# Performance work log

Measured on AMD Instinct MI355X. Metric: run time of the kernel, lower is better.

Reference implementation:

```python
import jax, jax.numpy as jnp
import numpy as np

N_NODES = 100000
N_EDGES = 600000
N_GRAPHS = 512
F_IN = 128
F_HID = 128
F_OUT = 128


def setup_inputs() -> dict:
    key = jax.random.key(0)
    ks = jax.random.split(key, 10)
    x = jax.random.normal(ks[0], (N_NODES, F_IN), dtype=jnp.float32)
    edge_index = jax.random.randint(ks[1], (2, N_EDGES), 0, N_NODES, dtype=jnp.int64)
    batch = jnp.sort(jax.random.randint(ks[2], (N_NODES,), 0, N_GRAPHS, dtype=jnp.int64))
    s1 = 1.0 / np.sqrt(F_IN)
    s2 = 1.0 / np.sqrt(F_HID)
    s3 = 1.0 / np.sqrt(F_OUT)
    W1 = jax.random.uniform(ks[3], (F_IN, F_HID), jnp.float32, -s1, s1)
    b1 = jnp.zeros((F_HID,), jnp.float32)
    W2 = jax.random.uniform(ks[4], (F_HID, F_OUT), jnp.float32, -s2, s2)
    b2 = jnp.zeros((F_OUT,), jnp.float32)
    Wlin = jax.random.uniform(ks[5], (F_OUT, 1), jnp.float32, -s3, s3)
    blin = jax.random.uniform(ks[6], (1,), jnp.float32, -s3, s3)
    return {"x": x, "edge_index": edge_index, "batch": batch,
            "W1": W1, "b1": b1, "W2": W2, "b2": b2, "Wlin": Wlin, "blin": blin}


def reference(x, edge_index, batch, W1, b1, W2, b2, Wlin, blin):
    N = x.shape[0]
    # GCN normalization with self-loops: D^{-1/2} (A + I) D^{-1/2}
    loop = jnp.arange(N, dtype=edge_index.dtype)
    src = jnp.concatenate([edge_index[0], loop])  # [E + N]
    dst = jnp.concatenate([edge_index[1], loop])
    deg = jax.ops.segment_sum(jnp.ones_like(dst, dtype=x.dtype), dst, num_segments=N)
    dis = jnp.where(deg > 0, jax.lax.rsqrt(jnp.maximum(deg, 1.0)), 0.0)  # deg^{-1/2}
    norm = (dis[src] * dis[dst])[:, None]  # [E+N, 1] edge weights

    def gcn_conv(h, W, b):
        hW = h @ W                                      # [N, d_out]
        msgs = norm * hW[src]                           # gather + scale
        agg = jax.ops.segment_sum(msgs, dst, num_segments=N)  # scatter-add
        return agg + b

    h = jax.nn.relu(gcn_conv(x, W1, b1))
    h = gcn_conv(h, W2, b2)

    # global_mean_pool over graph ids
    counts = jax.ops.segment_sum(jnp.ones((N,), x.dtype), batch, num_segments=N_GRAPHS)
    pooled = jax.ops.segment_sum(h, batch, num_segments=N_GRAPHS)
    pooled = pooled / jnp.maximum(counts, 1.0)[:, None]  # [N_GRAPHS, F_OUT]

    # dropout is identity in eval mode
    return pooled @ Wlin + blin  # [N_GRAPHS, 1]
```

## Files before the change

kernel.cpp:

```cpp
#include <hip/hip_runtime.h>

#define F 128
#define CAP 32

typedef _Float16 f16x8 __attribute__((ext_vector_type(8)));
typedef float f32x4 __attribute__((ext_vector_type(4)));

__global__ __launch_bounds__(256) void k_gemm_mfma(const float* __restrict__ X,
                                                   const float* __restrict__ W1,
                                                   int* __restrict__ cnt,
                                                   _Float16* __restrict__ Yb, int N) {
    __shared__ _Float16 Bs[F * F];

    int tid = threadIdx.x;
    int g = blockIdx.x;

    int zrow = g * 128 + tid;
    if (tid < 128 && zrow < N) cnt[zrow] = 0;

    {
        int krow = tid >> 1;
        int n0 = (tid & 1) * 64;
        int t = krow >> 5, j = krow & 7, qa = (krow >> 3) & 3;
        const float* wp = &W1[krow * F + n0];
#pragma unroll
        for (int q4 = 0; q4 < 16; ++q4) {
            float4 w = *(const float4*)(wp + q4 * 4);
            int n = n0 + q4 * 4;
            int c = n >> 4;
            int m = n & 15;
            int ob = (t * 8 + c) * 512 + j;
            Bs[ob + (qa * 16 + m + 0) * 8] = (_Float16)w.x;
            Bs[ob + (qa * 16 + m + 1) * 8] = (_Float16)w.y;
            Bs[ob + (qa * 16 + m + 2) * 8] = (_Float16)w.z;
            Bs[ob + (qa * 16 + m + 3) * 8] = (_Float16)w.w;
        }
    }
    __syncthreads();

    int lane = tid & 63, wave = tid >> 6;
    int quad = lane >> 4, m = lane & 15;
    int r0 = g * 128 + wave * 32;

    f32x4 acc[2][8];
#pragma unroll
    for (int rt = 0; rt < 2; ++rt)
#pragma unroll
        for (int c = 0; c < 8; ++c) acc[rt][c] = (f32x4)0.0f;

    int ra = r0 + m;      if (ra >= N) ra = N - 1;
    int rb = r0 + 16 + m; if (rb >= N) rb = N - 1;
    const float* pxa = &X[(size_t)ra * F + quad * 8];
    const float* pxb = &X[(size_t)rb * F + quad * 8];

    float4 a0 = *(const float4*)pxa, a1 = *(const float4*)(pxa + 4);
    float4 a2 = *(const float4*)pxb, a3 = *(const float4*)(pxb + 4);

#pragma unroll 1
    for (int t = 0; t < 4; ++t) {
        const _Float16* bp = &Bs[t * 4096 + lane * 8];
        f16x8 B[8];
#pragma unroll
        for (int c = 0; c < 8; ++c) B[c] = *(const f16x8*)(bp + c * 512);

        float fa[8] = {a0.x, a0.y, a0.z, a0.w, a1.x, a1.y, a1.z, a1.w};
        float fb[8] = {a2.x, a2.y, a2.z, a2.w, a3.x, a3.y, a3.z, a3.w};
        f16x8 A0, A1;
#pragma unroll
        for (int j = 0; j < 8; ++j) {
            A0[j] = (_Float16)fa[j];
            A1[j] = (_Float16)fb[j];
        }
        if (t < 3) {
            a0 = *(const float4*)(pxa + (t + 1) * 32);
            a1 = *(const float4*)(pxa + (t + 1) * 32 + 4);
            a2 = *(const float4*)(pxb + (t + 1) * 32);
            a3 = *(const float4*)(pxb + (t + 1) * 32 + 4);
        }
#pragma unroll
        for (int c = 0; c < 8; ++c) {
            acc[0][c] = __builtin_amdgcn_mfma_f32_16x16x32_f16(A0, B[c], acc[0][c], 0, 0, 0);
            acc[1][c] = __builtin_amdgcn_mfma_f32_16x16x32_f16(A1, B[c], acc[1][c], 0, 0, 0);
        }
    }

#pragma unroll
    for (int rt = 0; rt < 2; ++rt) {
        int rbase = r0 + rt * 16 + quad * 4;
#pragma unroll
        for (int rr = 0; rr < 4; ++rr) {
            int row = rbase + rr;
            if (row < N) {
#pragma unroll
                for (int c = 0; c < 8; ++c)
                    Yb[(size_t)row * F + c * 16 + m] = (_Float16)acc[rt][c][rr];
            }
        }
    }
}

__global__ __launch_bounds__(256) void k_prep(const float* __restrict__ W2, const float* __restrict__ Wlin,
                                              const float* __restrict__ b2, const float* __restrict__ blin,
                                              const int* __restrict__ batch,
                                              const int* __restrict__ src, const int* __restrict__ dst,
                                              float* __restrict__ w2l, float* __restrict__ cconst,
                                              int* __restrict__ gstart, int* __restrict__ cnt,
                                              int* __restrict__ srcs, int N, int E, int G, int bG) {
    int bid = blockIdx.x;
    int tid = threadIdx.x;
    if (bid == 0) {
        __shared__ float sh[F];
        if (tid < F) {
            float s = 0.0f;
            for (int j = 0; j < F; j += 4) {
                float4 w = *(const float4*)&W2[tid * F + j];
                float4 l = *(const float4*)&Wlin[j];
                s += w.x * l.x + w.y * l.y + w.z * l.z + w.w * l.w;
            }
            w2l[tid] = s;
            sh[tid] = b2[tid] * Wlin[tid];
        }
        __syncthreads();
        if (tid == 0) {
            float c = blin[0];
            for (int j = 0; j < F; ++j) c += sh[j];
            *cconst = c;
        }
    } else if (bid <= bG) {
        int g = (bid - 1) * 256 + tid;
        if (g < G) {
            int lo = 0, hi = N;
            while (lo < hi) { int mid = (lo + hi) >> 1; if (batch[mid] < g) lo = mid + 1; else hi = mid; }
            gstart[g] = lo;
            if (g == 0) gstart[G] = N;
        }
    } else {
        int e = (bid - 1 - bG) * 256 + tid;
        if (e < E) {
            int s = src[e], d = dst[e];
            int slot = atomicAdd(&cnt[d], 1);
            if (slot < CAP) srcs[d * CAP + slot] = s;
        }
    }
}

__global__ __launch_bounds__(256) void k_agg_z(const _Float16* __restrict__ hWb,
                                               const int* __restrict__ cnt, const int* __restrict__ srcs,
                                               const float* __restrict__ bias, const float* __restrict__ w2l,
                                               float* __restrict__ zt, int N) {
    __shared__ int sdeg[32], snode[32], smapN[32], smapD[32];
    int tid = threadIdx.x;
    int nb = blockIdx.x * 32;
    if (tid < 32) {
        int n = nb + tid;
        sdeg[tid]  = (n < N) ? cnt[n] : 0x40000000;
        snode[tid] = (n < N) ? n : -1;
    }
    __syncthreads();
    if (tid < 32) {
        int v = sdeg[tid];
        int rank = 0;
#pragma unroll 8
        for (int j = 0; j < 32; ++j) {
            int vj = sdeg[j];
            rank += (vj < v) || (vj == v && j < tid);
        }
        smapN[rank] = snode[tid];
        smapD[rank] = sdeg[tid];
    }
    __syncthreads();
    int node = smapN[tid >> 3];
    if (node < 0) return;
    int dg = smapD[tid >> 3];
    float di = rsqrtf((float)dg + 1.0f);
    int lane = tid & 7;
    float s[16];
    {
        const _Float16* pr = &hWb[(size_t)node * F + lane * 16];
        f16x8 v0 = *(const f16x8*)pr;
        f16x8 v1 = *(const f16x8*)(pr + 8);
#pragma unroll
        for (int j = 0; j < 8; ++j) { s[j] = di * (float)v0[j]; s[8 + j] = di * (float)v1[j]; }
    }
    int du = min(dg, CAP);
    int e0 = node * CAP, e1 = e0 + du;
    int e = e0;
    for (; e + 4 <= e1; e += 4) {
        int i0 = srcs[e], i1 = srcs[e + 1], i2 = srcs[e + 2], i3 = srcs[e + 3];
        float w0 = rsqrtf((float)cnt[i0] + 1.0f);
        float w1 = rsqrtf((float)cnt[i1] + 1.0f);
        float w2 = rsqrtf((float)cnt[i2] + 1.0f);
        float w3 = rsqrtf((float)cnt[i3] + 1.0f);
        const _Float16* p0 = &hWb[(size_t)i0 * F + lane * 16];
        const _Float16* p1 = &hWb[(size_t)i1 * F + lane * 16];
        const _Float16* p2 = &hWb[(size_t)i2 * F + lane * 16];
        const _Float16* p3 = &hWb[(size_t)i3 * F + lane * 16];
        f16x8 a0 = *(const f16x8*)p0, b0 = *(const f16x8*)(p0 + 8);
        f16x8 a1 = *(const f16x8*)p1, b1 = *(const f16x8*)(p1 + 8);
        f16x8 a2 = *(const f16x8*)p2, b2 = *(const f16x8*)(p2 + 8);
        f16x8 a3 = *(const f16x8*)p3, b3 = *(const f16x8*)(p3 + 8);
#pragma unroll
        for (int j = 0; j < 8; ++j) {
            s[j]     = fmaf(w0, (float)a0[j], s[j]);
            s[j]     = fmaf(w1, (float)a1[j], s[j]);
            s[j]     = fmaf(w2, (float)a2[j], s[j]);
            s[j]     = fmaf(w3, (float)a3[j], s[j]);
            s[8 + j] = fmaf(w0, (float)b0[j], s[8 + j]);
            s[8 + j] = fmaf(w1, (float)b1[j], s[8 + j]);
            s[8 + j] = fmaf(w2, (float)b2[j], s[8 + j]);
            s[8 + j] = fmaf(w3, (float)b3[j], s[8 + j]);
        }
    }
    for (; e < e1; ++e) {
        int i0 = srcs[e];
        float w0 = rsqrtf((float)cnt[i0] + 1.0f);
        const _Float16* pr = &hWb[(size_t)i0 * F + lane * 16];
        f16x8 v0 = *(const f16x8*)pr;
        f16x8 v1 = *(const f16x8*)(pr + 8);
#pragma unroll
        for (int j = 0; j < 8; ++j) {
            s[j]     = fmaf(w0, (float)v0[j], s[j]);
            s[8 + j] = fmaf(w0, (float)v1[j], s[8 + j]);
        }
    }
    float p = 0.0f;
#pragma unroll
    for (int q = 0; q < 4; ++q) {
        float4 bb = *(const float4*)&bias[lane * 16 + q * 4];
        float4 ww = *(const float4*)&w2l[lane * 16 + q * 4];
        p += fmaxf(fmaf(di, s[q * 4 + 0], bb.x), 0.0f) * ww.x;
        p += fmaxf(fmaf(di, s[q * 4 + 1], bb.y), 0.0f) * ww.y;
        p += fmaxf(fmaf(di, s[q * 4 + 2], bb.z), 0.0f) * ww.z;
        p += fmaxf(fmaf(di, s[q * 4 + 3], bb.w), 0.0f) * ww.w;
    }
#pragma unroll
    for (int d = 1; d < 8; d <<= 1) p += __shfl_xor(p, d);
    if (lane == 0) zt[node] = di * p;
}

__global__ __launch_bounds__(256) void k_pool(const float* __restrict__ zt,
                                              const int* __restrict__ cnt, const int* __restrict__ srcs,
                                              const int* __restrict__ gstart, const float* __restrict__ cconst,
                                              const float* __restrict__ blin, float* __restrict__ out, int G) {
    int g = blockIdx.x;
    int g0 = gstart[g], g1 = gstart[g + 1];
    float acc = 0.0f;
    for (int n = g0 + threadIdx.x; n < g1; n += 256) {
        float s = zt[n];
        int dg = cnt[n];
        int du = min(dg, CAP);
        int e0 = n * CAP, e1 = e0 + du;
        int e = e0;
        for (; e + 4 <= e1; e += 4) {
            s += zt[srcs[e]] + zt[srcs[e + 1]] + zt[srcs[e + 2]] + zt[srcs[e + 3]];
        }
        for (; e < e1; ++e) s += zt[srcs[e]];
        acc += rsqrtf((float)dg + 1.0f) * s;
    }
#pragma unroll
    for (int d = 1; d < 64; d <<= 1) acc += __shfl_xor(acc, d);
    __shared__ float ws4[4];
    if ((threadIdx.x & 63) == 0) ws4[threadIdx.x >> 6] = acc;
    __syncthreads();
    if (threadIdx.x == 0) {
        float sum = ws4[0] + ws4[1] + ws4[2] + ws4[3];
        int c = g1 - g0;
        out[g] = (c > 0) ? (sum / (float)c + cconst[0]) : blin[0];
    }
}


extern "C" void kernel_launch(void* const* d_in, const int* in_sizes, int n_in,
                              void* d_out, int out_size, void* d_ws, size_t ws_size,
                              hipStream_t stream) {
    const float* x    = (const float*)d_in[0];
    const int*   ei   = (const int*)d_in[1];
    const int*   batch= (const int*)d_in[2];
    const float* W1   = (const float*)d_in[3];
    const float* b1   = (const float*)d_in[4];
    const float* W2   = (const float*)d_in[5];
    const float* b2   = (const float*)d_in[6];
    const float* Wlin = (const float*)d_in[7];
    const float* blin = (const float*)d_in[8];
    float* out = (float*)d_out;

    const int N = in_sizes[2];
    const int E = in_sizes[1] / 2;
    const int G = out_size;
    const int* src = ei;
    const int* dst = ei + E;

    char* p = (char*)d_ws;
    auto take = [&](size_t bytes) { char* q = p; p += (bytes + 255) & ~(size_t)255; return q; };
    _Float16* hWb  = (_Float16*)take((size_t)N * F * 2);
    float*  ztbuf  = (float*)take((size_t)N * 4);
    int*    cnt    = (int*)  take((size_t)N * 4);
    int*    srcs   = (int*)  take((size_t)N * CAP * 4);
    int*    gstart = (int*)  take((size_t)(G + 1) * 4);
    float*  w2l    = (float*)take((size_t)F * 4);
    float*  cconst = (float*)take(256);

    const int bG  = (G + 255) / 256;
    const int nbGemm = (N + 127) / 128;
    const int nbE = (E + 255) / 256;

    k_gemm_mfma<<<nbGemm, 256, 0, stream>>>(x, W1, cnt, hWb, N);
    k_prep <<<1 + bG + nbE, 256, 0, stream>>>(W2, Wlin, b2, blin, batch, src, dst,
                                              w2l, cconst, gstart, cnt, srcs, N, E, G, bG);
    k_agg_z<<<(N + 31) / 32, 256, 0, stream>>>(hWb, cnt, srcs, b1, w2l, ztbuf, N);
    k_pool <<<G, 256, 0, stream>>>(ztbuf, cnt, srcs, gstart, cconst, blin, out, G);
}
```

Before: 183.3 us.

## Fuse all stages into one persistent kernel with software grid barriers

Merges the four kernels (GEMM, prep/edge scatter, aggregation, pooling) into one persistent kernel of a fixed 512-block grid. Stages are separated by an atomic-counter grid barrier, and each stage uses grid-stride loops. The aim is to remove the per-launch overhead and the gaps between launches. In exchange, the grid only works if all blocks are resident at once, concurrency drops during the gather-heavy aggregation phase, and the GEMM tiles split unevenly across the 512 blocks. A memset launch is also added to reset the barrier counter.

```diff
diff --git a/kernel.cpp b/kernel.cpp
--- a/kernel.cpp
+++ b/kernel.cpp
@@ -2,21 +2,77 @@
 
 #define F 128
 #define CAP 32
+#define GRID 512
 
 typedef _Float16 f16x8 __attribute__((ext_vector_type(8)));
 typedef float f32x4 __attribute__((ext_vector_type(4)));
 
-__global__ __launch_bounds__(256) void k_gemm_mfma(const float* __restrict__ X,
-                                                   const float* __restrict__ W1,
-                                                   int* __restrict__ cnt,
-                                                   _Float16* __restrict__ Yb, int N) {
+__device__ __forceinline__ void gridbar(int* bar, int target) {
+    __syncthreads();
+    if (threadIdx.x == 0) {
+        __threadfence();
+        atomicAdd(bar, 1);
+        while (__hip_atomic_load(bar, __ATOMIC_ACQUIRE, __HIP_MEMORY_SCOPE_AGENT) < target)
+            __builtin_amdgcn_s_sleep(2);
+        __threadfence();
+    }
+    __syncthreads();
+}
+
+__global__ __launch_bounds__(256, 4) void k_all(const float* __restrict__ X, const float* __restrict__ W1,
+                                                const float* __restrict__ W2, const float* __restrict__ Wlin,
+                                                const float* __restrict__ b1, const float* __restrict__ b2,
+                                                const float* __restrict__ blin, const int* __restrict__ batch,
+                                                const int* __restrict__ src, const int* __restrict__ dst,
+                                                int* __restrict__ cnt, int* __restrict__ srcs,
+                                                _Float16* __restrict__ hWb, float* __restrict__ w2l,
+                                                float* __restrict__ cconst, int* __restrict__ gstart,
+                                                float* __restrict__ zt, float* __restrict__ out,
+                                                int* __restrict__ bar,
+                                                int N, int E, int G, int nbGemm) {
+    int bid = blockIdx.x, tid = threadIdx.x;
+    const int gsz = GRID;
+
     __shared__ _Float16 Bs[F * F];
-
-    int tid = threadIdx.x;
-    int g = blockIdx.x;
-
-    int zrow = g * 128 + tid;
-    if (tid < 128 && zrow < N) cnt[zrow] = 0;
+    __shared__ float sh[F];
+    __shared__ int sdeg[32], snode[32], smapN[32], smapD[32];
+    __shared__ float ws4[4];
+
+    {
+        int i = (bid * 256 + tid) * 4;
+        if (i + 3 < N) {
+            *(int4*)&cnt[i] = make_int4(0, 0, 0, 0);
+        } else {
+            for (int j = i; j < N; ++j) cnt[j] = 0;
+        }
+    }
+
+    if (bid == 0) {
+        if (tid < F) {
+            float s = 0.0f;
+            for (int j = 0; j < F; j += 4) {
+                float4 w = *(const float4*)&W2[tid * F + j];
+                float4 l = *(const float4*)&Wlin[j];
+                s += w.x * l.x + w.y * l.y + w.z * l.z + w.w * l.w;
+            }
+            w2l[tid] = s;
+            sh[tid] = b2[tid] * Wlin[tid];
+        }
+        __syncthreads();
+        if (tid == 0) {
+            float c = blin[0];
+            for (int j = 0; j < F; ++j) c += sh[j];
+            *cconst = c;
+        }
+    } else if (bid <= (G + 255) / 256) {
+        int g = (bid - 1) * 256 + tid;
+        if (g < G) {
+            int lo = 0, hi = N;
+            while (lo < hi) { int mid = (lo + hi) >> 1; if (batch[mid] < g) lo = mid + 1; else hi = mid; }
+            gstart[g] = lo;
+            if (g == 0) gstart[G] = N;
+        }
+    }
 
     {
         int krow = tid >> 1;
@@ -38,234 +94,198 @@
     }
     __syncthreads();
 
-    int lane = tid & 63, wave = tid >> 6;
-    int quad = lane >> 4, m = lane & 15;
-    int r0 = g * 128 + wave * 32;
-
-    f32x4 acc[2][8];
-#pragma unroll
-    for (int rt = 0; rt < 2; ++rt)
-#pragma unroll
-        for (int c = 0; c < 8; ++c) acc[rt][c] = (f32x4)0.0f;
-
-    int ra = r0 + m;      if (ra >= N) ra = N - 1;
-    int rb = r0 + 16 + m; if (rb >= N) rb = N - 1;
-    const float* pxa = &X[(size_t)ra * F + quad * 8];
-    const float* pxb = &X[(size_t)rb * F + quad * 8];
-
-    float4 a0 = *(const float4*)pxa, a1 = *(const float4*)(pxa + 4);
-    float4 a2 = *(const float4*)pxb, a3 = *(const float4*)(pxb + 4);
+    for (int tile = bid; tile < nbGemm; tile += gsz) {
+        int lane = tid & 63, wave = tid >> 6;
+        int quad = lane >> 4, m = lane & 15;
+        int r0 = tile * 128 + wave * 32;
+
+        f32x4 acc[2][8];
+#pragma unroll
+        for (int rt = 0; rt < 2; ++rt)
+#pragma unroll
+            for (int c = 0; c < 8; ++c) acc[rt][c] = (f32x4)0.0f;
+
+        int ra = r0 + m;      if (ra >= N) ra = N - 1;
+        int rb = r0 + 16 + m; if (rb >= N) rb = N - 1;
+        const float* pxa = &X[(size_t)ra * F + quad * 8];
+        const float* pxb = &X[(size_t)rb * F + quad * 8];
+
+        float4 a0 = *(const float4*)pxa, a1 = *(const float4*)(pxa + 4);
+        float4 a2 = *(const float4*)pxb, a3 = *(const float4*)(pxb + 4);
 
 #pragma unroll 1
-    for (int t = 0; t < 4; ++t) {
-        const _Float16* bp = &Bs[t * 4096 + lane * 8];
-        f16x8 B[8];
-#pragma unroll
-        for (int c = 0; c < 8; ++c) B[c] = *(const f16x8*)(bp + c * 512);
-
-        float fa[8] = {a0.x, a0.y, a0.z, a0.w, a1.x, a1.y, a1.z, a1.w};
-        float fb[8] = {a2.x, a2.y, a2.z, a2.w, a3.x, a3.y, a3.z, a3.w};
-        f16x8 A0, A1;
-#pragma unroll
-        for (int j = 0; j < 8; ++j) {
-            A0[j] = (_Float16)fa[j];
-            A1[j] = (_Float16)fb[j];
-        }
-        if (t < 3) {
-            a0 = *(const float4*)(pxa + (t + 1) * 32);
-            a1 = *(const float4*)(pxa + (t + 1) * 32 + 4);
-            a2 = *(const float4*)(pxb + (t + 1) * 32);
-            a3 = *(const float4*)(pxb + (t + 1) * 32 + 4);
-        }
-#pragma unroll
-        for (int c = 0; c < 8; ++c) {
-            acc[0][c] = __builtin_amdgcn_mfma_f32_16x16x32_f16(A0, B[c], acc[0][c], 0, 0, 0);
-            acc[1][c] = __builtin_amdgcn_mfma_f32_16x16x32_f16(A1, B[c], acc[1][c], 0, 0, 0);
-        }
-    }
-
-#pragma unroll
-    for (int rt = 0; rt < 2; ++rt) {
-        int rbase = r0 + rt * 16 + quad * 4;
-#pragma unroll
-        for (int rr = 0; rr < 4; ++rr) {
-            int row = rbase + rr;
-            if (row < N) {
-#pragma unroll
-                for (int c = 0; c < 8; ++c)
-                    Yb[(size_t)row * F + c * 16 + m] = (_Float16)acc[rt][c][rr];
-            }
-        }
-    }
-}
-
-__global__ __launch_bounds__(256) void k_prep(const float* __restrict__ W2, const float* __restrict__ Wlin,
-                                              const float* __restrict__ b2, const float* __restrict__ blin,
-                                              const int* __restrict__ batch,
-                                              const int* __restrict__ src, const int* __restrict__ dst,
-                                              float* __restrict__ w2l, float* __restrict__ cconst,
-                                              int* __restrict__ gstart, int* __restrict__ cnt,
-                                              int* __restrict__ srcs, int N, int E, int G, int bG) {
-    int bid = blockIdx.x;
-    int tid = threadIdx.x;
-    if (bid == 0) {
-        __shared__ float sh[F];
-        if (tid < F) {
-            float s = 0.0f;
-            for (int j = 0; j < F; j += 4) {
-                float4 w = *(const float4*)&W2[tid * F + j];
-                float4 l = *(const float4*)&Wlin[j];
-                s += w.x * l.x + w.y * l.y + w.z * l.z + w.w * l.w;
-            }
-            w2l[tid] = s;
-            sh[tid] = b2[tid] * Wlin[tid];
-        }
+        for (int t = 0; t < 4; ++t) {
+            const _Float16* bp = &Bs[t * 4096 + lane * 8];
+            f16x8 B[8];
+#pragma unroll
+            for (int c = 0; c < 8; ++c) B[c] = *(const f16x8*)(bp + c * 512);
+
+            float fa[8] = {a0.x, a0.y, a0.z, a0.w, a1.x, a1.y, a1.z, a1.w};
+            float fb[8] = {a2.x, a2.y, a2.z, a2.w, a3.x, a3.y, a3.z, a3.w};
+            f16x8 A0, A1;
+#pragma unroll
+            for (int j = 0; j < 8; ++j) {
+                A0[j] = (_Float16)fa[j];
+                A1[j] = (_Float16)fb[j];
+            }
+            if (t < 3) {
+                a0 = *(const float4*)(pxa + (t + 1) * 32);
+                a1 = *(const float4*)(pxa + (t + 1) * 32 + 4);
+                a2 = *(const float4*)(pxb + (t + 1) * 32);
+                a3 = *(const float4*)(pxb + (t + 1) * 32 + 4);
+            }
+#pragma unroll
+            for (int c = 0; c < 8; ++c) {
+                acc[0][c] = __builtin_amdgcn_mfma_f32_16x16x32_f16(A0, B[c], acc[0][c], 0, 0, 0);
+                acc[1][c] = __builtin_amdgcn_mfma_f32_16x16x32_f16(A1, B[c], acc[1][c], 0, 0, 0);
+            }
+        }
+
+#pragma unroll
+        for (int rt = 0; rt < 2; ++rt) {
+            int rbase = r0 + rt * 16 + quad * 4;
+#pragma unroll
+            for (int rr = 0; rr < 4; ++rr) {
+                int row = rbase + rr;
+                if (row < N) {
+#pragma unroll
+                    for (int c = 0; c < 8; ++c)
+                        hWb[(size_t)row * F + c * 16 + m] = (_Float16)acc[rt][c][rr];
+                }
+            }
+        }
+    }
+
+    gridbar(bar, gsz);
+
+    for (int e = bid * 256 + tid; e < E; e += gsz * 256) {
+        int s = src[e], d = dst[e];
+        int slot = atomicAdd(&cnt[d], 1);
+        if (slot < CAP) srcs[d * CAP + slot] = s;
+    }
+
+    gridbar(bar, 2 * gsz);
+
+    {
+        int ngroups = (N + 31) >> 5;
+        for (int u = bid; u < ngroups; u += gsz) {
+            int nb = u * 32;
+            if (tid < 32) {
+                int n = nb + tid;
+                sdeg[tid]  = (n < N) ? cnt[n] : 0x40000000;
+                snode[tid] = (n < N) ? n : -1;
+            }
+            __syncthreads();
+            if (tid < 32) {
+                int v = sdeg[tid];
+                int rank = 0;
+#pragma unroll 8
+                for (int j = 0; j < 32; ++j) {
+                    int vj = sdeg[j];
+                    rank += (vj < v) || (vj == v && j < tid);
+                }
+                smapN[rank] = snode[tid];
+                smapD[rank] = sdeg[tid];
+            }
+            __syncthreads();
+            int node = smapN[tid >> 3];
+            int dg = smapD[tid >> 3];
+            bool valid = (node >= 0);
+            int nodeSafe = valid ? node : 0;
+            float di = rsqrtf((float)dg + 1.0f);
+            int lane = tid & 7;
+            float s[16];
+            {
+                const _Float16* pr = &hWb[(size_t)nodeSafe * F + lane * 16];
+                f16x8 v0 = *(const f16x8*)pr;
+                f16x8 v1 = *(const f16x8*)(pr + 8);
+#pragma unroll
+                for (int j = 0; j < 8; ++j) { s[j] = di * (float)v0[j]; s[8 + j] = di * (float)v1[j]; }
+            }
+            int du = valid ? min(dg, CAP) : 0;
+            int e0 = nodeSafe * CAP, e1 = e0 + du;
+            int e = e0;
+            for (; e + 4 <= e1; e += 4) {
+                int i0 = srcs[e], i1 = srcs[e + 1], i2 = srcs[e + 2], i3 = srcs[e + 3];
+                float w0 = rsqrtf((float)cnt[i0] + 1.0f);
+                float w1 = rsqrtf((float)cnt[i1] + 1.0f);
+                float w2 = rsqrtf((float)cnt[i2] + 1.0f);
+                float w3 = rsqrtf((float)cnt[i3] + 1.0f);
+                const _Float16* p0 = &hWb[(size_t)i0 * F + lane * 16];
+                const _Float16* p1 = &hWb[(size_t)i1 * F + lane * 16];
+                const _Float16* p2 = &hWb[(size_t)i2 * F + lane * 16];
+                const _Float16* p3 = &hWb[(size_t)i3 * F + lane * 16];
+                f16x8 a0 = *(const f16x8*)p0, b0v = *(const f16x8*)(p0 + 8);
+                f16x8 a1 = *(const f16x8*)p1, b1v = *(const f16x8*)(p1 + 8);
+                f16x8 a2 = *(const f16x8*)p2, b2v = *(const f16x8*)(p2 + 8);
+                f16x8 a3 = *(const f16x8*)p3, b3v = *(const f16x8*)(p3 + 8);
+#pragma unroll
+                for (int j = 0; j < 8; ++j) {
+                    s[j]     = fmaf(w0, (float)a0[j], s[j]);
+                    s[j]     = fmaf(w1, (float)a1[j], s[j]);
+                    s[j]     = fmaf(w2, (float)a2[j], s[j]);
+                    s[j]     = fmaf(w3, (float)a3[j], s[j]);
+                    s[8 + j] = fmaf(w0, (float)b0v[j], s[8 + j]);
+                    s[8 + j] = fmaf(w1, (float)b1v[j], s[8 + j]);
+                    s[8 + j] = fmaf(w2, (float)b2v[j], s[8 + j]);
+                    s[8 + j] = fmaf(w3, (float)b3v[j], s[8 + j]);
+                }
+            }
+            for (; e < e1; ++e) {
+                int i0 = srcs[e];
+                float w0 = rsqrtf((float)cnt[i0] + 1.0f);
+                const _Float16* pr = &hWb[(size_t)i0 * F + lane * 16];
+                f16x8 v0 = *(const f16x8*)pr;
+                f16x8 v1 = *(const f16x8*)(pr + 8);
+#pragma unroll
+                for (int j = 0; j < 8; ++j) {
+                    s[j]     = fmaf(w0, (float)v0[j], s[j]);
+                    s[8 + j] = fmaf(w0, (float)v1[j], s[8 + j]);
+                }
+            }
+            float p = 0.0f;
+#pragma unroll
+            for (int q = 0; q < 4; ++q) {
+                float4 bb = *(const float4*)&b1[lane * 16 + q * 4];
+                float4 ww = *(const float4*)&w2l[lane * 16 + q * 4];
+                p += fmaxf(fmaf(di, s[q * 4 + 0], bb.x), 0.0f) * ww.x;
+                p += fmaxf(fmaf(di, s[q * 4 + 1], bb.y), 0.0f) * ww.y;
+                p += fmaxf(fmaf(di, s[q * 4 + 2], bb.z), 0.0f) * ww.z;
+                p += fmaxf(fmaf(di, s[q * 4 + 3], bb.w), 0.0f) * ww.w;
+            }
+#pragma unroll
+            for (int d = 1; d < 8; d <<= 1) p += __shfl_xor(p, d);
+            if (valid && lane == 0) zt[node] = di * p;
+        }
+    }
+
+    gridbar(bar, 3 * gsz);
+
+    for (int g = bid; g < G; g += gsz) {
+        int g0 = gstart[g], g1 = gstart[g + 1];
+        float acc = 0.0f;
+        for (int n = g0 + tid; n < g1; n += 256) {
+            float s = zt[n];
+            int dg = cnt[n];
+            int du = min(dg, CAP);
+            int e0 = n * CAP, e1 = e0 + du;
+            int e = e0;
+            for (; e + 4 <= e1; e += 4) {
+                s += zt[srcs[e]] + zt[srcs[e + 1]] + zt[srcs[e + 2]] + zt[srcs[e + 3]];
+            }
+            for (; e < e1; ++e) s += zt[srcs[e]];
+            acc += rsqrtf((float)dg + 1.0f) * s;
+        }
+#pragma unroll
+        for (int d = 1; d < 64; d <<= 1) acc += __shfl_xor(acc, d);
+        if ((tid & 63) == 0) ws4[tid >> 6] = acc;
         __syncthreads();
         if (tid == 0) {
-            float c = blin[0];
-            for (int j = 0; j < F; ++j) c += sh[j];
-            *cconst = c;
-        }
-    } else if (bid <= bG) {
-        int g = (bid - 1) * 256 + tid;
-        if (g < G) {
-            int lo = 0, hi = N;
-            while (lo < hi) { int mid = (lo + hi) >> 1; if (batch[mid] < g) lo = mid + 1; else hi = mid; }
-            gstart[g] = lo;
-            if (g == 0) gstart[G] = N;
-        }
-    } else {
-        int e = (bid - 1 - bG) * 256 + tid;
-        if (e < E) {
-            int s = src[e], d = dst[e];
-            int slot = atomicAdd(&cnt[d], 1);
-            if (slot < CAP) srcs[d * CAP + slot] = s;
-        }
-    }
-}
-
-__global__ __launch_bounds__(256) void k_agg_z(const _Float16* __restrict__ hWb,
-                                               const int* __restrict__ cnt, const int* __restrict__ srcs,
-                                               const float* __restrict__ bias, const float* __restrict__ w2l,
-                                               float* __restrict__ zt, int N) {
-    __shared__ int sdeg[32], snode[32], smapN[32], smapD[32];
-    int tid = threadIdx.x;
-    int nb = blockIdx.x * 32;
-    if (tid < 32) {
-        int n = nb + tid;
-        sdeg[tid]  = (n < N) ? cnt[n] : 0x40000000;
-        snode[tid] = (n < N) ? n : -1;
-    }
-    __syncthreads();
-    if (tid < 32) {
-        int v = sdeg[tid];
-        int rank = 0;
-#pragma unroll 8
-        for (int j = 0; j < 32; ++j) {
-            int vj = sdeg[j];
-            rank += (vj < v) || (vj == v && j < tid);
-        }
-        smapN[rank] = snode[tid];
-        smapD[rank] = sdeg[tid];
-    }
-    __syncthreads();
-    int node = smapN[tid >> 3];
-    if (node < 0) return;
-    int dg = smapD[tid >> 3];
-    float di = rsqrtf((float)dg + 1.0f);
-    int lane = tid & 7;
-    float s[16];
-    {
-        const _Float16* pr = &hWb[(size_t)node * F + lane * 16];
-        f16x8 v0 = *(const f16x8*)pr;
-        f16x8 v1 = *(const f16x8*)(pr + 8);
-#pragma unroll
-        for (int j = 0; j < 8; ++j) { s[j] = di * (float)v0[j]; s[8 + j] = di * (float)v1[j]; }
-    }
-    int du = min(dg, CAP);
-    int e0 = node * CAP, e1 = e0 + du;
-    int e = e0;
-    for (; e + 4 <= e1; e += 4) {
-        int i0 = srcs[e], i1 = srcs[e + 1], i2 = srcs[e + 2], i3 = srcs[e + 3];
-        float w0 = rsqrtf((float)cnt[i0] + 1.0f);
-        float w1 = rsqrtf((float)cnt[i1] + 1.0f);
-        float w2 = rsqrtf((float)cnt[i2] + 1.0f);
-        float w3 = rsqrtf((float)cnt[i3] + 1.0f);
-        const _Float16* p0 = &hWb[(size_t)i0 * F + lane * 16];
-        const _Float16* p1 = &hWb[(size_t)i1 * F + lane * 16];
-        const _Float16* p2 = &hWb[(size_t)i2 * F + lane * 16];
-        const _Float16* p3 = &hWb[(size_t)i3 * F + lane * 16];
-        f16x8 a0 = *(const f16x8*)p0, b0 = *(const f16x8*)(p0 + 8);
-        f16x8 a1 = *(const f16x8*)p1, b1 = *(const f16x8*)(p1 + 8);
-        f16x8 a2 = *(const f16x8*)p2, b2 = *(const f16x8*)(p2 + 8);
-        f16x8 a3 = *(const f16x8*)p3, b3 = *(const f16x8*)(p3 + 8);
-#pragma unroll
-        for (int j = 0; j < 8; ++j) {
-            s[j]     = fmaf(w0, (float)a0[j], s[j]);
-            s[j]     = fmaf(w1, (float)a1[j], s[j]);
-            s[j]     = fmaf(w2, (float)a2[j], s[j]);
-            s[j]     = fmaf(w3, (float)a3[j], s[j]);
-            s[8 + j] = fmaf(w0, (float)b0[j], s[8 + j]);
-            s[8 + j] = fmaf(w1, (float)b1[j], s[8 + j]);
-            s[8 + j] = fmaf(w2, (float)b2[j], s[8 + j]);
-            s[8 + j] = fmaf(w3, (float)b3[j], s[8 + j]);
-        }
-    }
-    for (; e < e1; ++e) {
-        int i0 = srcs[e];
-        float w0 = rsqrtf((float)cnt[i0] + 1.0f);
-        const _Float16* pr = &hWb[(size_t)i0 * F + lane * 16];
-        f16x8 v0 = *(const f16x8*)pr;
-        f16x8 v1 = *(const f16x8*)(pr + 8);
-#pragma unroll
-        for (int j = 0; j < 8; ++j) {
-            s[j]     = fmaf(w0, (float)v0[j], s[j]);
-            s[8 + j] = fmaf(w0, (float)v1[j], s[8 + j]);
-        }
-    }
-    float p = 0.0f;
-#pragma unroll
-    for (int q = 0; q < 4; ++q) {
-        float4 bb = *(const float4*)&bias[lane * 16 + q * 4];
-        float4 ww = *(const float4*)&w2l[lane * 16 + q * 4];
-        p += fmaxf(fmaf(di, s[q * 4 + 0], bb.x), 0.0f) * ww.x;
-        p += fmaxf(fmaf(di, s[q * 4 + 1], bb.y), 0.0f) * ww.y;
-        p += fmaxf(fmaf(di, s[q * 4 + 2], bb.z), 0.0f) * ww.z;
-        p += fmaxf(fmaf(di, s[q * 4 + 3], bb.w), 0.0f) * ww.w;
-    }
-#pragma unroll
-    for (int d = 1; d < 8; d <<= 1) p += __shfl_xor(p, d);
-    if (lane == 0) zt[node] = di * p;
-}
-
-__global__ __launch_bounds__(256) void k_pool(const float* __restrict__ zt,
-                                              const int* __restrict__ cnt, const int* __restrict__ srcs,
-                                              const int* __restrict__ gstart, const float* __restrict__ cconst,
-                                              const float* __restrict__ blin, float* __restrict__ out, int G) {
-    int g = blockIdx.x;
-    int g0 = gstart[g], g1 = gstart[g + 1];
-    float acc = 0.0f;
-    for (int n = g0 + threadIdx.x; n < g1; n += 256) {
-        float s = zt[n];
-        int dg = cnt[n];
-        int du = min(dg, CAP);
-        int e0 = n * CAP, e1 = e0 + du;
-        int e = e0;
-        for (; e + 4 <= e1; e += 4) {
-            s += zt[srcs[e]] + zt[srcs[e + 1]] + zt[srcs[e + 2]] + zt[srcs[e + 3]];
-        }
-        for (; e < e1; ++e) s += zt[srcs[e]];
-        acc += rsqrtf((float)dg + 1.0f) * s;
-    }
-#pragma unroll
-    for (int d = 1; d < 64; d <<= 1) acc += __shfl_xor(acc, d);
-    __shared__ float ws4[4];
-    if ((threadIdx.x & 63) == 0) ws4[threadIdx.x >> 6] = acc;
-    __syncthreads();
-    if (threadIdx.x == 0) {
-        float sum = ws4[0] + ws4[1] + ws4[2] + ws4[3];
-        int c = g1 - g0;
-        out[g] = (c > 0) ? (sum / (float)c + cconst[0]) : blin[0];
+            float sum = ws4[0] + ws4[1] + ws4[2] + ws4[3];
+            int c = g1 - g0;
+            out[g] = (c > 0) ? (sum / (float)c + cconst[0]) : blin[0];
+        }
+        __syncthreads();
     }
 }
 
@@ -284,9 +304,9 @@
     const float* blin = (const float*)d_in[8];
     float* out = (float*)d_out;
 
-    const int N = in_sizes[2];
-    const int E = in_sizes[1] / 2;
-    const int G = out_size;
+    int N = in_sizes[2];
+    int E = in_sizes[1] / 2;
+    int G = out_size;
     const int* src = ei;
     const int* dst = ei + E;
 
@@ -299,14 +319,12 @@
     int*    gstart = (int*)  take((size_t)(G + 1) * 4);
     float*  w2l    = (float*)take((size_t)F * 4);
     float*  cconst = (float*)take(256);
-
-    const int bG  = (G + 255) / 256;
-    const int nbGemm = (N + 127) / 128;
-    const int nbE = (E + 255) / 256;
-
-    k_gemm_mfma<<<nbGemm, 256, 0, stream>>>(x, W1, cnt, hWb, N);
-    k_prep <<<1 + bG + nbE, 256, 0, stream>>>(W2, Wlin, b2, blin, batch, src, dst,
-                                              w2l, cconst, gstart, cnt, srcs, N, E, G, bG);
-    k_agg_z<<<(N + 31) / 32, 256, 0, stream>>>(hWb, cnt, srcs, b1, w2l, ztbuf, N);
-    k_pool <<<G, 256, 0, stream>>>(ztbuf, cnt, srcs, gstart, cconst, blin, out, G);
+    int*    bar    = (int*)  take(256);
+
+    int nbGemm = (N + 127) / 128;
+
+    hipMemsetAsync(bar, 0, 4, stream);
+    k_all<<<GRID, 256, 0, stream>>>(x, W1, W2, Wlin, b1, b2, blin, batch, src, dst,
+                                    cnt, srcs, hWb, w2l, cconst, gstart, ztbuf, out,
+                                    bar, N, E, G, nbGemm);
 }
```

Measured after the change: 519.0 us. 183% more time.
